# Kernel tuning notes

Hardware: AMD Instinct MI355X
Metric: run time of the kernel (lower is better)

Reference implementation:

```python
import jax, jax.numpy as jnp
import numpy as np

T, B, H, D = 128, 8, 8, 64


def setup_inputs() -> dict:
    key = jax.random.key(0)
    kA, kB, kS = jax.random.split(key, 3)
    # Gated-delta transition matrices: near-identity contractions so the
    # length-T matrix-product recurrence is numerically stable, mimicking
    # A_t = gamma_t * (I - beta_t k_t k_t^T) of the gated delta rule.
    eye = jnp.eye(D, dtype=jnp.float32)
    A = 0.9 * eye + 0.06 * jax.random.normal(kA, (T, B, H, D, D), dtype=jnp.float32)
    Bm = jax.random.normal(kB, (T, B, H, D, D), dtype=jnp.float32)
    init_state = jax.random.normal(kS, (B, H, D, D), dtype=jnp.float32)
    return {"A": A, "Bm": Bm, "init_state": init_state}


def reference(A, Bm, init_state):
    """Gated delta rule recurrence S_t = S_{t-1} @ A_t + B_t for all t,
    computed with a parallel associative scan (Blelloch-equivalent).

    A:  [T,B,H,D,D] transition matrices
    Bm: [T,B,H,D,D] additive updates
    init_state: [B,H,D,D]
    returns states: [T,B,H,D,D]
    """
    def combine(e1, e2):
        # apply e1 first, then e2:
        # (S A1 + B1) A2 + B2 = S (A1 A2) + (B1 A2 + B2)
        A1, B1 = e1
        A2, B2 = e2
        A12 = jnp.einsum('tbhij,tbhjk->tbhik', A1, A2)
        B12 = jnp.einsum('tbhij,tbhjk->tbhik', B1, A2) + B2
        return (A12, B12)

    cumA, cumB = jax.lax.associative_scan(combine, (A, Bm), axis=0)
    # S_t = init_state @ cumA_t + cumB_t
    states = jnp.einsum('bhij,tbhjk->tbhik', init_state, cumA) + cumB
    return states
```

## Files before the change

### kernel.cpp

```cpp
#include <hip/hip_runtime.h>


constexpr int kT = 128;
constexpr int kBH = 64;
constexpr int kD = 64;
constexpr int kTile = kD * kD;

typedef __attribute__((ext_vector_type(8))) short short8;
typedef __attribute__((ext_vector_type(4))) short short4v;
typedef __attribute__((ext_vector_type(4))) float f32x4;

__device__ __forceinline__ unsigned short f2bf(float f) {
  unsigned int u = __float_as_uint(f);
  u += 0x7FFFu + ((u >> 16) & 1u);
  return (unsigned short)(u >> 16);
}
__device__ __forceinline__ float bf2f(unsigned short h) {
  return __uint_as_float(((unsigned int)h) << 16);
}
__device__ __forceinline__ int swzi(int r, int c) { return (r * 64 + c) ^ ((r & 7) << 3); }

__device__ __forceinline__ f32x4 mfma16(short8 a, short8 b, f32x4 c) {
  return __builtin_amdgcn_mfma_f32_16x16x32_bf16(a, b, c, 0, 0, 0);
}

__device__ __forceinline__ void split4(const f32x4 v, short4v& h, short4v& l) {
#pragma unroll
  for (int i = 0; i < 4; ++i) {
    const unsigned short hh = f2bf(v[i]);
    h[i] = (short)hh;
    l[i] = (short)f2bf(v[i] - bf2f(hh));
  }
}

__global__ __launch_bounds__(256, 2) void gdr_fold(
    const float* __restrict__ srcA, const float* __restrict__ srcB,
    float* __restrict__ dstA, float* __restrict__ dstB,
    int perChain, long chainBase, long idxBase, long elemStride, int nElem) {
  __shared__ unsigned short sAh[4096], sAl[4096];
  __shared__ unsigned short sPAh[4096], sPAl[4096];
  __shared__ unsigned short sPBh[4096], sPBl[4096];

  const int tid = threadIdx.x;
  const int lane = tid & 63, wave = tid >> 6;
  const int wr = wave >> 1, wc = wave & 1;
  const int q = lane >> 4, l15 = lane & 15;
  const int bh = blockIdx.x / perChain, id = blockIdx.x % perChain;
  const long e0 = (long)bh * chainBase + (long)id * idxBase;
  const int an = lane, akb = wave;

  f32x4 apa[2][2], apb[2][2];
  {
    const float* At = srcA + (size_t)e0 * kTile;
    const float* Bt = srcB + (size_t)e0 * kTile;
#pragma unroll
    for (int mi = 0; mi < 2; ++mi)
#pragma unroll
      for (int ni = 0; ni < 2; ++ni) {
        const int off = (wc * 32 + ni * 16 + l15) * 64 + wr * 32 + mi * 16 + q * 4;
        apa[mi][ni] = *reinterpret_cast<const f32x4*>(At + off);
        apb[mi][ni] = *reinterpret_cast<const f32x4*>(Bt + off);
      }
  }

  float pfA[16];
  f32x4 pfB[2][2];
  {
    const float* At = srcA + (size_t)(e0 + elemStride) * kTile;
    const float* Bt = srcB + (size_t)(e0 + elemStride) * kTile;
#pragma unroll
    for (int kk = 0; kk < 16; ++kk) pfA[kk] = At[(akb * 16 + kk) * 64 + an];
#pragma unroll
    for (int mi = 0; mi < 2; ++mi)
#pragma unroll
      for (int ni = 0; ni < 2; ++ni)
        pfB[mi][ni] = *reinterpret_cast<const f32x4*>(
            Bt + (wc * 32 + ni * 16 + l15) * 64 + wr * 32 + mi * 16 + q * 4);
  }

  for (int i = 1; i < nElem; ++i) {
    if (i > 1) __syncthreads();
#pragma unroll
    for (int mi = 0; mi < 2; ++mi)
#pragma unroll
      for (int ni = 0; ni < 2; ++ni) {
        const int b = wc * 32 + ni * 16 + l15;
        const int a0 = wr * 32 + mi * 16 + q * 4;
        const int idx = swzi(b, a0);
        short4v h, l;
        split4(apa[mi][ni], h, l);
        *reinterpret_cast<short4v*>(&sPAh[idx]) = h;
        *reinterpret_cast<short4v*>(&sPAl[idx]) = l;
        split4(apb[mi][ni], h, l);
        *reinterpret_cast<short4v*>(&sPBh[idx]) = h;
        *reinterpret_cast<short4v*>(&sPBl[idx]) = l;
      }
#pragma unroll
    for (int s = 0; s < 2; ++s) {
      short8 h, l;
#pragma unroll
      for (int j = 0; j < 8; ++j) {
        const float v = pfA[s * 8 + j];
        const unsigned short hh = f2bf(v);
        h[j] = (short)hh;
        l[j] = (short)f2bf(v - bf2f(hh));
      }
      const int idx = swzi(an, akb * 16 + s * 8);
      *reinterpret_cast<short8*>(&sAh[idx]) = h;
      *reinterpret_cast<short8*>(&sAl[idx]) = l;
    }
    __syncthreads();

#pragma unroll
    for (int mi = 0; mi < 2; ++mi)
#pragma unroll
      for (int ni = 0; ni < 2; ++ni) {
        apa[mi][ni] = (f32x4){0.f, 0.f, 0.f, 0.f};
        apb[mi][ni] = pfB[mi][ni];
      }

    const int in = (i + 1 < nElem) ? i + 1 : i;
    {
      const float* At = srcA + (size_t)(e0 + (long)in * elemStride) * kTile;
      const float* Bt = srcB + (size_t)(e0 + (long)in * elemStride) * kTile;
#pragma unroll
      for (int kk = 0; kk < 16; ++kk) pfA[kk] = At[(akb * 16 + kk) * 64 + an];
#pragma unroll
      for (int mi = 0; mi < 2; ++mi)
#pragma unroll
        for (int ni = 0; ni < 2; ++ni)
          pfB[mi][ni] = *reinterpret_cast<const f32x4*>(
              Bt + (wc * 32 + ni * 16 + l15) * 64 + wr * 32 + mi * 16 + q * 4);
    }

#pragma unroll
    for (int ks = 0; ks < 2; ++ks) {
      short8 xh[2], xl[2], yah[2], yal[2], ybh[2], ybl[2];
      const int colb = ks * 32 + q * 8;
#pragma unroll
      for (int mi = 0; mi < 2; ++mi) {
        const int idx = swzi(wr * 32 + mi * 16 + l15, colb);
        xh[mi] = *reinterpret_cast<const short8*>(&sAh[idx]);
        xl[mi] = *reinterpret_cast<const short8*>(&sAl[idx]);
      }
#pragma unroll
      for (int ni = 0; ni < 2; ++ni) {
        const int idx = swzi(wc * 32 + ni * 16 + l15, colb);
        yah[ni] = *reinterpret_cast<const short8*>(&sPAh[idx]);
        yal[ni] = *reinterpret_cast<const short8*>(&sPAl[idx]);
        ybh[ni] = *reinterpret_cast<const short8*>(&sPBh[idx]);
        ybl[ni] = *reinterpret_cast<const short8*>(&sPBl[idx]);
      }
#pragma unroll
      for (int mi = 0; mi < 2; ++mi)
#pragma unroll
        for (int ni = 0; ni < 2; ++ni) {
          apa[mi][ni] = mfma16(xh[mi], yah[ni], apa[mi][ni]);
          apa[mi][ni] = mfma16(xh[mi], yal[ni], apa[mi][ni]);
          apa[mi][ni] = mfma16(xl[mi], yah[ni], apa[mi][ni]);
          apb[mi][ni] = mfma16(xh[mi], ybh[ni], apb[mi][ni]);
          apb[mi][ni] = mfma16(xh[mi], ybl[ni], apb[mi][ni]);
          apb[mi][ni] = mfma16(xl[mi], ybh[ni], apb[mi][ni]);
        }
    }
  }

  float* pao = dstA + (size_t)blockIdx.x * kTile;
  float* pbo = dstB + (size_t)blockIdx.x * kTile;
#pragma unroll
  for (int mi = 0; mi < 2; ++mi)
#pragma unroll
    for (int ni = 0; ni < 2; ++ni) {
      const int off = (wc * 32 + ni * 16 + l15) * 64 + wr * 32 + mi * 16 + q * 4;
      *reinterpret_cast<f32x4*>(pao + off) = apa[mi][ni];
      *reinterpret_cast<f32x4*>(pbo + off) = apb[mi][ni];
    }
}

__global__ __launch_bounds__(256, 2) void gdr_scan(
    const float* __restrict__ srcA, const float* __restrict__ srcB,
    const float* __restrict__ S0, float* __restrict__ out,
    int perChain, long chainBase, long idxBase, long elemStride,
    int nSteps, int tbMul, int tStep) {
  __shared__ unsigned short sAh[4096], sAl[4096];
  __shared__ unsigned short sSh[4096], sSl[4096];

  const int tid = threadIdx.x;
  const int lane = tid & 63, wave = tid >> 6;
  const int wr = wave >> 1, wc = wave & 1;
  const int q = lane >> 4, l15 = lane & 15;
  const int bh = blockIdx.x / perChain, id = blockIdx.x % perChain;
  const long e0 = (long)bh * chainBase + (long)id * idxBase;
  const int tBase = id * tbMul;
  const int an = lane, akb = wave;

  f32x4 acc[2][2];
  {
    const float* Sb = (tBase == 0) ? (S0 + (size_t)bh * kTile)
                                   : (out + ((size_t)(tBase - 1) * kBH + bh) * kTile);
#pragma unroll
    for (int mi = 0; mi < 2; ++mi)
#pragma unroll
      for (int ni = 0; ni < 2; ++ni)
        acc[mi][ni] = *reinterpret_cast<const f32x4*>(
            Sb + (wc * 32 + ni * 16 + l15) * 64 + wr * 32 + mi * 16 + q * 4);
  }

  float pfA[16];
  f32x4 pfB[2][2];
  {
    const float* At = srcA + (size_t)e0 * kTile;
    const float* Bt = srcB + (size_t)e0 * kTile;
#pragma unroll
    for (int kk = 0; kk < 16; ++kk) pfA[kk] = At[(akb * 16 + kk) * 64 + an];
#pragma unroll
    for (int mi = 0; mi < 2; ++mi)
#pragma unroll
      for (int ni = 0; ni < 2; ++ni)
        pfB[mi][ni] = *reinterpret_cast<const f32x4*>(
            Bt + (wc * 32 + ni * 16 + l15) * 64 + wr * 32 + mi * 16 + q * 4);
  }

  for (int i = 0; i < nSteps; ++i) {
    if (i) __syncthreads();
#pragma unroll
    for (int mi = 0; mi < 2; ++mi)
#pragma unroll
      for (int ni = 0; ni < 2; ++ni) {
        const int b = wc * 32 + ni * 16 + l15;
        const int a0 = wr * 32 + mi * 16 + q * 4;
        const int idx = swzi(b, a0);
        short4v h, l;
        split4(acc[mi][ni], h, l);
        *reinterpret_cast<short4v*>(&sSh[idx]) = h;
        *reinterpret_cast<short4v*>(&sSl[idx]) = l;
      }
#pragma unroll
    for (int s = 0; s < 2; ++s) {
      short8 h, l;
#pragma unroll
      for (int j = 0; j < 8; ++j) {
        const float v = pfA[s * 8 + j];
        const unsigned short hh = f2bf(v);
        h[j] = (short)hh;
        l[j] = (short)f2bf(v - bf2f(hh));
      }
      const int idx = swzi(an, akb * 16 + s * 8);
      *reinterpret_cast<short8*>(&sAh[idx]) = h;
      *reinterpret_cast<short8*>(&sAl[idx]) = l;
    }
    __syncthreads();

#pragma unroll
    for (int mi = 0; mi < 2; ++mi)
#pragma unroll
      for (int ni = 0; ni < 2; ++ni)
        acc[mi][ni] = pfB[mi][ni];

    const int in = (i + 1 < nSteps) ? i + 1 : i;
    {
      const float* At = srcA + (size_t)(e0 + (long)in * elemStride) * kTile;
      const float* Bt = srcB + (size_t)(e0 + (long)in * elemStride) * kTile;
#pragma unroll
      for (int kk = 0; kk < 16; ++kk) pfA[kk] = At[(akb * 16 + kk) * 64 + an];
#pragma unroll
      for (int mi = 0; mi < 2; ++mi)
#pragma unroll
        for (int ni = 0; ni < 2; ++ni)
          pfB[mi][ni] = *reinterpret_cast<const f32x4*>(
              Bt + (wc * 32 + ni * 16 + l15) * 64 + wr * 32 + mi * 16 + q * 4);
    }

#pragma unroll
    for (int ks = 0; ks < 2; ++ks) {
      short8 xh[2], xl[2], yh[2], yl[2];
      const int colb = ks * 32 + q * 8;
#pragma unroll
      for (int mi = 0; mi < 2; ++mi) {
        const int idx = swzi(wr * 32 + mi * 16 + l15, colb);
        xh[mi] = *reinterpret_cast<const short8*>(&sAh[idx]);
        xl[mi] = *reinterpret_cast<const short8*>(&sAl[idx]);
      }
#pragma unroll
      for (int ni = 0; ni < 2; ++ni) {
        const int idx = swzi(wc * 32 + ni * 16 + l15, colb);
        yh[ni] = *reinterpret_cast<const short8*>(&sSh[idx]);
        yl[ni] = *reinterpret_cast<const short8*>(&sSl[idx]);
      }
#pragma unroll
      for (int mi = 0; mi < 2; ++mi)
#pragma unroll
        for (int ni = 0; ni < 2; ++ni) {
          acc[mi][ni] = mfma16(xh[mi], yh[ni], acc[mi][ni]);
          acc[mi][ni] = mfma16(xh[mi], yl[ni], acc[mi][ni]);
          acc[mi][ni] = mfma16(xl[mi], yh[ni], acc[mi][ni]);
        }
    }

    const int t = tBase + (i + 1) * tStep - 1;
    float* o = out + ((size_t)t * kBH + bh) * kTile;
#pragma unroll
    for (int mi = 0; mi < 2; ++mi)
#pragma unroll
      for (int ni = 0; ni < 2; ++ni) {
        const int off = (wc * 32 + ni * 16 + l15) * 64 + wr * 32 + mi * 16 + q * 4;
        *reinterpret_cast<f32x4*>(o + off) = acc[mi][ni];
      }
  }
}

extern "C" void kernel_launch(void* const* d_in, const int* in_sizes, int n_in,
                              void* d_out, int out_size, void* d_ws, size_t ws_size,
                              hipStream_t stream) {
  const float* A  = (const float*)d_in[0];
  const float* Bm = (const float*)d_in[1];
  const float* S0 = (const float*)d_in[2];
  float* out = (float*)d_out;

  int NC;
  if (ws_size >= (size_t)5120 * kTile * 4)      NC = 32;
  else if (ws_size >= (size_t)2560 * kTile * 4) NC = 16;
  else                                          NC = 8;
  const int CH = kT / NC;
  const int NG = NC / 4;

  float* PA = (float*)d_ws;
  float* PB = PA + (size_t)kBH * NC * kTile;
  float* GA = PB + (size_t)kBH * NC * kTile;
  float* GB = GA + (size_t)kBH * NG * kTile;

  gdr_fold<<<dim3(kBH * NC), dim3(256), 0, stream>>>(
      A, Bm, PA, PB, NC, 1L, (long)CH * kBH, (long)kBH, CH);
  gdr_fold<<<dim3(kBH * NG), dim3(256), 0, stream>>>(
      PA, PB, GA, GB, NG, (long)NC, 4L, 1L, 4);
  gdr_scan<<<dim3(kBH), dim3(256), 0, stream>>>(
      GA, GB, S0, out, 1, (long)NG, 0L, 1L, NG, 0, 4 * CH);
  gdr_scan<<<dim3(kBH * NG), dim3(256), 0, stream>>>(
      PA, PB, S0, out, NG, (long)NC, 4L, 1L, 3, 4 * CH, CH);
  gdr_scan<<<dim3(kBH * NC), dim3(256), 0, stream>>>(
      A, Bm, S0, out, NC, 1L, (long)CH * kBH, (long)kBH, CH - 1, CH, 1);
}
```

Baseline: 184.7 us.

## Restructure scan into two-level hierarchy with register-resident state and double-buffered A

```diff
diff --git a/kernel.cpp b/kernel.cpp
--- a/kernel.cpp
+++ b/kernel.cpp
@@ -5,307 +5,251 @@
 constexpr int kBH = 64;
 constexpr int kD = 64;
 constexpr int kTile = kD * kD;
+constexpr int kNC = 16;
+constexpr int kCH = 8;
 
 typedef __attribute__((ext_vector_type(8))) short short8;
-typedef __attribute__((ext_vector_type(4))) short short4v;
 typedef __attribute__((ext_vector_type(4))) float f32x4;
-
-__device__ __forceinline__ unsigned short f2bf(float f) {
-  unsigned int u = __float_as_uint(f);
-  u += 0x7FFFu + ((u >> 16) & 1u);
-  return (unsigned short)(u >> 16);
-}
-__device__ __forceinline__ float bf2f(unsigned short h) {
-  return __uint_as_float(((unsigned int)h) << 16);
-}
+using u32 = unsigned int;
+
+union U8 { u32 u[4]; short8 s; };
+
 __device__ __forceinline__ int swzi(int r, int c) { return (r * 64 + c) ^ ((r & 7) << 3); }
 
 __device__ __forceinline__ f32x4 mfma16(short8 a, short8 b, f32x4 c) {
   return __builtin_amdgcn_mfma_f32_16x16x32_bf16(a, b, c, 0, 0, 0);
 }
 
-__device__ __forceinline__ void split4(const f32x4 v, short4v& h, short4v& l) {
-#pragma unroll
-  for (int i = 0; i < 4; ++i) {
-    const unsigned short hh = f2bf(v[i]);
-    h[i] = (short)hh;
-    l[i] = (short)f2bf(v[i] - bf2f(hh));
-  }
-}
-
-__global__ __launch_bounds__(256, 2) void gdr_fold(
+__device__ __forceinline__ void pk_split(float a, float b, u32& h, u32& l) {
+  u32 hu;
+  asm("v_cvt_pk_bf16_f32 %0, %1, %2" : "=v"(hu) : "v"(a), "v"(b));
+  const float ra = a - __uint_as_float(hu << 16);
+  const float rb = b - __uint_as_float(hu & 0xffff0000u);
+  u32 lu;
+  asm("v_cvt_pk_bf16_f32 %0, %1, %2" : "=v"(lu) : "v"(ra), "v"(rb));
+  h = hu;
+  l = lu;
+}
+
+__device__ __forceinline__ short8 gather_frag(u32 p01, u32 p23, u32 q01, u32 q23,
+                                              int ad0, int ad1, bool lowh) {
+  U8 r;
+  int x, y;
+  x = __builtin_amdgcn_ds_bpermute(ad0, (int)p01);
+  y = __builtin_amdgcn_ds_bpermute(ad0, (int)q01);
+  r.u[0] = (u32)(lowh ? x : y);
+  x = __builtin_amdgcn_ds_bpermute(ad0, (int)p23);
+  y = __builtin_amdgcn_ds_bpermute(ad0, (int)q23);
+  r.u[1] = (u32)(lowh ? x : y);
+  x = __builtin_amdgcn_ds_bpermute(ad1, (int)p01);
+  y = __builtin_amdgcn_ds_bpermute(ad1, (int)q01);
+  r.u[2] = (u32)(lowh ? x : y);
+  x = __builtin_amdgcn_ds_bpermute(ad1, (int)p23);
+  y = __builtin_amdgcn_ds_bpermute(ad1, (int)q23);
+  r.u[3] = (u32)(lowh ? x : y);
+  return r.s;
+}
+
+__device__ __forceinline__ void load_pfA(float* pfA, const float* At, int lane, int w) {
+#pragma unroll
+  for (int kk = 0; kk < 16; ++kk) pfA[kk] = At[(w * 16 + kk) * 64 + lane];
+}
+__device__ __forceinline__ void load_pfB(f32x4* pfB, const float* Bt, int rowbase, int q) {
+#pragma unroll
+  for (int cm = 0; cm < 4; ++cm)
+    pfB[cm] = *reinterpret_cast<const f32x4*>(Bt + rowbase + cm * 16 + q * 4);
+}
+
+__device__ __forceinline__ void stage_A(unsigned short* Ah, unsigned short* Al,
+                                        const float* pfA, int lane, int w) {
+#pragma unroll
+  for (int s = 0; s < 2; ++s) {
+    U8 h, l;
+#pragma unroll
+    for (int p = 0; p < 4; ++p) {
+      u32 hu, lu;
+      pk_split(pfA[s * 8 + 2 * p], pfA[s * 8 + 2 * p + 1], hu, lu);
+      h.u[p] = hu;
+      l.u[p] = lu;
+    }
+    const int idx = swzi(lane, w * 16 + s * 8);
+    *reinterpret_cast<short8*>(&Ah[idx]) = h.s;
+    *reinterpret_cast<short8*>(&Al[idx]) = l.s;
+  }
+}
+
+__global__ __launch_bounds__(256, 3) void gdr_fold(
     const float* __restrict__ srcA, const float* __restrict__ srcB,
     float* __restrict__ dstA, float* __restrict__ dstB,
     int perChain, long chainBase, long idxBase, long elemStride, int nElem) {
-  __shared__ unsigned short sAh[4096], sAl[4096];
-  __shared__ unsigned short sPAh[4096], sPAl[4096];
-  __shared__ unsigned short sPBh[4096], sPBl[4096];
+  __shared__ unsigned short sAh[2][4096], sAl[2][4096];
 
   const int tid = threadIdx.x;
-  const int lane = tid & 63, wave = tid >> 6;
-  const int wr = wave >> 1, wc = wave & 1;
+  const int lane = tid & 63, w = tid >> 6;
   const int q = lane >> 4, l15 = lane & 15;
   const int bh = blockIdx.x / perChain, id = blockIdx.x % perChain;
   const long e0 = (long)bh * chainBase + (long)id * idxBase;
-  const int an = lane, akb = wave;
-
-  f32x4 apa[2][2], apb[2][2];
+  const int rowbase = (w * 16 + l15) * 64;
+  const int ad0 = (l15 + ((lane >> 4) & 1) * 32) * 4;
+  const int ad1 = ad0 + 64;
+  const bool lowh = lane < 32;
+  const int nS = nElem - 1;
+
+  f32x4 apa[4], apb[4];
   {
     const float* At = srcA + (size_t)e0 * kTile;
     const float* Bt = srcB + (size_t)e0 * kTile;
 #pragma unroll
-    for (int mi = 0; mi < 2; ++mi)
-#pragma unroll
-      for (int ni = 0; ni < 2; ++ni) {
-        const int off = (wc * 32 + ni * 16 + l15) * 64 + wr * 32 + mi * 16 + q * 4;
-        apa[mi][ni] = *reinterpret_cast<const f32x4*>(At + off);
-        apb[mi][ni] = *reinterpret_cast<const f32x4*>(Bt + off);
+    for (int cm = 0; cm < 4; ++cm) {
+      apa[cm] = *reinterpret_cast<const f32x4*>(At + rowbase + cm * 16 + q * 4);
+      apb[cm] = *reinterpret_cast<const f32x4*>(Bt + rowbase + cm * 16 + q * 4);
+    }
+  }
+
+  float pfA[16];
+  f32x4 pfB[4];
+  load_pfA(pfA, srcA + (size_t)(e0 + elemStride) * kTile, lane, w);
+  stage_A(sAh[0], sAl[0], pfA, lane, w);
+  __syncthreads();
+  {
+    const long e2 = e0 + (long)(nS > 1 ? 2 : 1) * elemStride;
+    load_pfA(pfA, srcA + (size_t)e2 * kTile, lane, w);
+    load_pfB(pfB, srcB + (size_t)(e0 + elemStride) * kTile, rowbase, q);
+  }
+
+  for (int j = 0; j < nS; ++j) {
+    const int cur = j & 1;
+    f32x4 npa[4], npb[4];
+#pragma unroll
+    for (int cm = 0; cm < 4; ++cm) {
+      npa[cm] = (f32x4){0.f, 0.f, 0.f, 0.f};
+      npb[cm] = pfB[cm];
+    }
+#pragma unroll
+    for (int ks = 0; ks < 2; ++ks) {
+      u32 pa01h, pa01l, pa23h, pa23l, qa01h, qa01l, qa23h, qa23l;
+      u32 pb01h, pb01l, pb23h, pb23l, qb01h, qb01l, qb23h, qb23l;
+      pk_split(apa[2 * ks][0], apa[2 * ks][1], pa01h, pa01l);
+      pk_split(apa[2 * ks][2], apa[2 * ks][3], pa23h, pa23l);
+      pk_split(apa[2 * ks + 1][0], apa[2 * ks + 1][1], qa01h, qa01l);
+      pk_split(apa[2 * ks + 1][2], apa[2 * ks + 1][3], qa23h, qa23l);
+      pk_split(apb[2 * ks][0], apb[2 * ks][1], pb01h, pb01l);
+      pk_split(apb[2 * ks][2], apb[2 * ks][3], pb23h, pb23l);
+      pk_split(apb[2 * ks + 1][0], apb[2 * ks + 1][1], qb01h, qb01l);
+      pk_split(apb[2 * ks + 1][2], apb[2 * ks + 1][3], qb23h, qb23l);
+      const short8 bah = gather_frag(pa01h, pa23h, qa01h, qa23h, ad0, ad1, lowh);
+      const short8 bal = gather_frag(pa01l, pa23l, qa01l, qa23l, ad0, ad1, lowh);
+      const short8 bbh = gather_frag(pb01h, pb23h, qb01h, qb23h, ad0, ad1, lowh);
+      const short8 bbl = gather_frag(pb01l, pb23l, qb01l, qb23l, ad0, ad1, lowh);
+#pragma unroll
+      for (int cm = 0; cm < 4; ++cm) {
+        const int ai = swzi(cm * 16 + l15, ks * 32 + q * 8);
+        const short8 ah = *reinterpret_cast<const short8*>(&sAh[cur][ai]);
+        const short8 al = *reinterpret_cast<const short8*>(&sAl[cur][ai]);
+        npa[cm] = mfma16(ah, bah, npa[cm]);
+        npa[cm] = mfma16(ah, bal, npa[cm]);
+        npa[cm] = mfma16(al, bah, npa[cm]);
+        npb[cm] = mfma16(ah, bbh, npb[cm]);
+        npb[cm] = mfma16(ah, bbl, npb[cm]);
+        npb[cm] = mfma16(al, bbh, npb[cm]);
       }
-  }
-
-  float pfA[16];
-  f32x4 pfB[2][2];
-  {
-    const float* At = srcA + (size_t)(e0 + elemStride) * kTile;
-    const float* Bt = srcB + (size_t)(e0 + elemStride) * kTile;
-#pragma unroll
-    for (int kk = 0; kk < 16; ++kk) pfA[kk] = At[(akb * 16 + kk) * 64 + an];
-#pragma unroll
-    for (int mi = 0; mi < 2; ++mi)
-#pragma unroll
-      for (int ni = 0; ni < 2; ++ni)
-        pfB[mi][ni] = *reinterpret_cast<const f32x4*>(
-            Bt + (wc * 32 + ni * 16 + l15) * 64 + wr * 32 + mi * 16 + q * 4);
-  }
-
-  for (int i = 1; i < nElem; ++i) {
-    if (i > 1) __syncthreads();
-#pragma unroll
-    for (int mi = 0; mi < 2; ++mi)
-#pragma unroll
-      for (int ni = 0; ni < 2; ++ni) {
-        const int b = wc * 32 + ni * 16 + l15;
-        const int a0 = wr * 32 + mi * 16 + q * 4;
-        const int idx = swzi(b, a0);
-        short4v h, l;
-        split4(apa[mi][ni], h, l);
-        *reinterpret_cast<short4v*>(&sPAh[idx]) = h;
-        *reinterpret_cast<short4v*>(&sPAl[idx]) = l;
-        split4(apb[mi][ni], h, l);
-        *reinterpret_cast<short4v*>(&sPBh[idx]) = h;
-        *reinterpret_cast<short4v*>(&sPBl[idx]) = l;
-      }
-#pragma unroll
-    for (int s = 0; s < 2; ++s) {
-      short8 h, l;
-#pragma unroll
-      for (int j = 0; j < 8; ++j) {
-        const float v = pfA[s * 8 + j];
-        const unsigned short hh = f2bf(v);
-        h[j] = (short)hh;
-        l[j] = (short)f2bf(v - bf2f(hh));
-      }
-      const int idx = swzi(an, akb * 16 + s * 8);
-      *reinterpret_cast<short8*>(&sAh[idx]) = h;
-      *reinterpret_cast<short8*>(&sAl[idx]) = l;
-    }
-    __syncthreads();
-
-#pragma unroll
-    for (int mi = 0; mi < 2; ++mi)
-#pragma unroll
-      for (int ni = 0; ni < 2; ++ni) {
-        apa[mi][ni] = (f32x4){0.f, 0.f, 0.f, 0.f};
-        apb[mi][ni] = pfB[mi][ni];
-      }
-
-    const int in = (i + 1 < nElem) ? i + 1 : i;
-    {
-      const float* At = srcA + (size_t)(e0 + (long)in * elemStride) * kTile;
-      const float* Bt = srcB + (size_t)(e0 + (long)in * elemStride) * kTile;
-#pragma unroll
-      for (int kk = 0; kk < 16; ++kk) pfA[kk] = At[(akb * 16 + kk) * 64 + an];
-#pragma unroll
-      for (int mi = 0; mi < 2; ++mi)
-#pragma unroll
-        for (int ni = 0; ni < 2; ++ni)
-          pfB[mi][ni] = *reinterpret_cast<const f32x4*>(
-              Bt + (wc * 32 + ni * 16 + l15) * 64 + wr * 32 + mi * 16 + q * 4);
-    }
-
-#pragma unroll
-    for (int ks = 0; ks < 2; ++ks) {
-      short8 xh[2], xl[2], yah[2], yal[2], ybh[2], ybl[2];
-      const int colb = ks * 32 + q * 8;
-#pragma unroll
-      for (int mi = 0; mi < 2; ++mi) {
-        const int idx = swzi(wr * 32 + mi * 16 + l15, colb);
-        xh[mi] = *reinterpret_cast<const short8*>(&sAh[idx]);
-        xl[mi] = *reinterpret_cast<const short8*>(&sAl[idx]);
-      }
-#pragma unroll
-      for (int ni = 0; ni < 2; ++ni) {
-        const int idx = swzi(wc * 32 + ni * 16 + l15, colb);
-        yah[ni] = *reinterpret_cast<const short8*>(&sPAh[idx]);
-        yal[ni] = *reinterpret_cast<const short8*>(&sPAl[idx]);
-        ybh[ni] = *reinterpret_cast<const short8*>(&sPBh[idx]);
-        ybl[ni] = *reinterpret_cast<const short8*>(&sPBl[idx]);
-      }
-#pragma unroll
-      for (int mi = 0; mi < 2; ++mi)
-#pragma unroll
-        for (int ni = 0; ni < 2; ++ni) {
-          apa[mi][ni] = mfma16(xh[mi], yah[ni], apa[mi][ni]);
-          apa[mi][ni] = mfma16(xh[mi], yal[ni], apa[mi][ni]);
-          apa[mi][ni] = mfma16(xl[mi], yah[ni], apa[mi][ni]);
-          apb[mi][ni] = mfma16(xh[mi], ybh[ni], apb[mi][ni]);
-          apb[mi][ni] = mfma16(xh[mi], ybl[ni], apb[mi][ni]);
-          apb[mi][ni] = mfma16(xl[mi], ybh[ni], apb[mi][ni]);
-        }
-    }
+    }
+    if (j + 1 < nS) {
+      stage_A(sAh[cur ^ 1], sAl[cur ^ 1], pfA, lane, w);
+      const int ja = (j + 3 <= nS) ? j + 3 : nS;
+      load_pfA(pfA, srcA + (size_t)(e0 + (long)ja * elemStride) * kTile, lane, w);
+      load_pfB(pfB, srcB + (size_t)(e0 + (long)(j + 2) * elemStride) * kTile, rowbase, q);
+    }
+#pragma unroll
+    for (int cm = 0; cm < 4; ++cm) { apa[cm] = npa[cm]; apb[cm] = npb[cm]; }
+    if (j + 1 < nS) __syncthreads();
   }
 
   float* pao = dstA + (size_t)blockIdx.x * kTile;
   float* pbo = dstB + (size_t)blockIdx.x * kTile;
 #pragma unroll
-  for (int mi = 0; mi < 2; ++mi)
-#pragma unroll
-    for (int ni = 0; ni < 2; ++ni) {
-      const int off = (wc * 32 + ni * 16 + l15) * 64 + wr * 32 + mi * 16 + q * 4;
-      *reinterpret_cast<f32x4*>(pao + off) = apa[mi][ni];
-      *reinterpret_cast<f32x4*>(pbo + off) = apb[mi][ni];
-    }
-}
-
-__global__ __launch_bounds__(256, 2) void gdr_scan(
+  for (int cm = 0; cm < 4; ++cm) {
+    *reinterpret_cast<f32x4*>(pao + rowbase + cm * 16 + q * 4) = apa[cm];
+    *reinterpret_cast<f32x4*>(pbo + rowbase + cm * 16 + q * 4) = apb[cm];
+  }
+}
+
+__global__ __launch_bounds__(256, 4) void gdr_scan(
     const float* __restrict__ srcA, const float* __restrict__ srcB,
     const float* __restrict__ S0, float* __restrict__ out,
     int perChain, long chainBase, long idxBase, long elemStride,
     int nSteps, int tbMul, int tStep) {
-  __shared__ unsigned short sAh[4096], sAl[4096];
-  __shared__ unsigned short sSh[4096], sSl[4096];
+  __shared__ unsigned short sAh[2][4096], sAl[2][4096];
 
   const int tid = threadIdx.x;
-  const int lane = tid & 63, wave = tid >> 6;
-  const int wr = wave >> 1, wc = wave & 1;
+  const int lane = tid & 63, w = tid >> 6;
   const int q = lane >> 4, l15 = lane & 15;
   const int bh = blockIdx.x / perChain, id = blockIdx.x % perChain;
   const long e0 = (long)bh * chainBase + (long)id * idxBase;
   const int tBase = id * tbMul;
-  const int an = lane, akb = wave;
-
-  f32x4 acc[2][2];
+  const int rowbase = (w * 16 + l15) * 64;
+  const int ad0 = (l15 + ((lane >> 4) & 1) * 32) * 4;
+  const int ad1 = ad0 + 64;
+  const bool lowh = lane < 32;
+
+  f32x4 acc[4];
   {
     const float* Sb = (tBase == 0) ? (S0 + (size_t)bh * kTile)
                                    : (out + ((size_t)(tBase - 1) * kBH + bh) * kTile);
 #pragma unroll
-    for (int mi = 0; mi < 2; ++mi)
-#pragma unroll
-      for (int ni = 0; ni < 2; ++ni)
-        acc[mi][ni] = *reinterpret_cast<const f32x4*>(
-            Sb + (wc * 32 + ni * 16 + l15) * 64 + wr * 32 + mi * 16 + q * 4);
+    for (int cm = 0; cm < 4; ++cm)
+      acc[cm] = *reinterpret_cast<const f32x4*>(Sb + rowbase + cm * 16 + q * 4);
   }
 
   float pfA[16];
-  f32x4 pfB[2][2];
-  {
-    const float* At = srcA + (size_t)e0 * kTile;
-    const float* Bt = srcB + (size_t)e0 * kTile;
-#pragma unroll
-    for (int kk = 0; kk < 16; ++kk) pfA[kk] = At[(akb * 16 + kk) * 64 + an];
-#pragma unroll
-    for (int mi = 0; mi < 2; ++mi)
-#pragma unroll
-      for (int ni = 0; ni < 2; ++ni)
-        pfB[mi][ni] = *reinterpret_cast<const f32x4*>(
-            Bt + (wc * 32 + ni * 16 + l15) * 64 + wr * 32 + mi * 16 + q * 4);
+  f32x4 pfB[4];
+  load_pfA(pfA, srcA + (size_t)e0 * kTile, lane, w);
+  stage_A(sAh[0], sAl[0], pfA, lane, w);
+  __syncthreads();
+  {
+    const long e1 = e0 + (long)(nSteps > 1 ? 1 : 0) * elemStride;
+    load_pfA(pfA, srcA + (size_t)e1 * kTile, lane, w);
+    load_pfB(pfB, srcB + (size_t)e0 * kTile, rowbase, q);
   }
 
   for (int i = 0; i < nSteps; ++i) {
-    if (i) __syncthreads();
-#pragma unroll
-    for (int mi = 0; mi < 2; ++mi)
-#pragma unroll
-      for (int ni = 0; ni < 2; ++ni) {
-        const int b = wc * 32 + ni * 16 + l15;
-        const int a0 = wr * 32 + mi * 16 + q * 4;
-        const int idx = swzi(b, a0);
-        short4v h, l;
-        split4(acc[mi][ni], h, l);
-        *reinterpret_cast<short4v*>(&sSh[idx]) = h;
-        *reinterpret_cast<short4v*>(&sSl[idx]) = l;
+    const int cur = i & 1;
+    f32x4 nacc[4];
+#pragma unroll
+    for (int cm = 0; cm < 4; ++cm) nacc[cm] = pfB[cm];
+#pragma unroll
+    for (int ks = 0; ks < 2; ++ks) {
+      u32 p01h, p01l, p23h, p23l, q01h, q01l, q23h, q23l;
+      pk_split(acc[2 * ks][0], acc[2 * ks][1], p01h, p01l);
+      pk_split(acc[2 * ks][2], acc[2 * ks][3], p23h, p23l);
+      pk_split(acc[2 * ks + 1][0], acc[2 * ks + 1][1], q01h, q01l);
+      pk_split(acc[2 * ks + 1][2], acc[2 * ks + 1][3], q23h, q23l);
+      const short8 bfh = gather_frag(p01h, p23h, q01h, q23h, ad0, ad1, lowh);
+      const short8 bfl = gather_frag(p01l, p23l, q01l, q23l, ad0, ad1, lowh);
+#pragma unroll
+      for (int cm = 0; cm < 4; ++cm) {
+        const int ai = swzi(cm * 16 + l15, ks * 32 + q * 8);
+        const short8 ah = *reinterpret_cast<const short8*>(&sAh[cur][ai]);
+        const short8 al = *reinterpret_cast<const short8*>(&sAl[cur][ai]);
+        nacc[cm] = mfma16(ah, bfh, nacc[cm]);
+        nacc[cm] = mfma16(ah, bfl, nacc[cm]);
+        nacc[cm] = mfma16(al, bfh, nacc[cm]);
       }
-#pragma unroll
-    for (int s = 0; s < 2; ++s) {
-      short8 h, l;
-#pragma unroll
-      for (int j = 0; j < 8; ++j) {
-        const float v = pfA[s * 8 + j];
-        const unsigned short hh = f2bf(v);
-        h[j] = (short)hh;
-        l[j] = (short)f2bf(v - bf2f(hh));
-      }
-      const int idx = swzi(an, akb * 16 + s * 8);
-      *reinterpret_cast<short8*>(&sAh[idx]) = h;
-      *reinterpret_cast<short8*>(&sAl[idx]) = l;
-    }
-    __syncthreads();
-
-#pragma unroll
-    for (int mi = 0; mi < 2; ++mi)
-#pragma unroll
-      for (int ni = 0; ni < 2; ++ni)
-        acc[mi][ni] = pfB[mi][ni];
-
-    const int in = (i + 1 < nSteps) ? i + 1 : i;
-    {
-      const float* At = srcA + (size_t)(e0 + (long)in * elemStride) * kTile;
-      const float* Bt = srcB + (size_t)(e0 + (long)in * elemStride) * kTile;
-#pragma unroll
-      for (int kk = 0; kk < 16; ++kk) pfA[kk] = At[(akb * 16 + kk) * 64 + an];
-#pragma unroll
-      for (int mi = 0; mi < 2; ++mi)
-#pragma unroll
-        for (int ni = 0; ni < 2; ++ni)
-          pfB[mi][ni] = *reinterpret_cast<const f32x4*>(
-              Bt + (wc * 32 + ni * 16 + l15) * 64 + wr * 32 + mi * 16 + q * 4);
-    }
-
-#pragma unroll
-    for (int ks = 0; ks < 2; ++ks) {
-      short8 xh[2], xl[2], yh[2], yl[2];
-      const int colb = ks * 32 + q * 8;
-#pragma unroll
-      for (int mi = 0; mi < 2; ++mi) {
-        const int idx = swzi(wr * 32 + mi * 16 + l15, colb);
-        xh[mi] = *reinterpret_cast<const short8*>(&sAh[idx]);
-        xl[mi] = *reinterpret_cast<const short8*>(&sAl[idx]);
-      }
-#pragma unroll
-      for (int ni = 0; ni < 2; ++ni) {
-        const int idx = swzi(wc * 32 + ni * 16 + l15, colb);
-        yh[ni] = *reinterpret_cast<const short8*>(&sSh[idx]);
-        yl[ni] = *reinterpret_cast<const short8*>(&sSl[idx]);
-      }
-#pragma unroll
-      for (int mi = 0; mi < 2; ++mi)
-#pragma unroll
-        for (int ni = 0; ni < 2; ++ni) {
-          acc[mi][ni] = mfma16(xh[mi], yh[ni], acc[mi][ni]);
-          acc[mi][ni] = mfma16(xh[mi], yl[ni], acc[mi][ni]);
-          acc[mi][ni] = mfma16(xl[mi], yh[ni], acc[mi][ni]);
-        }
-    }
-
+    }
+    if (i + 1 < nSteps) {
+      stage_A(sAh[cur ^ 1], sAl[cur ^ 1], pfA, lane, w);
+      const int ia = (i + 2 <= nSteps - 1) ? i + 2 : nSteps - 1;
+      load_pfA(pfA, srcA + (size_t)(e0 + (long)ia * elemStride) * kTile, lane, w);
+      load_pfB(pfB, srcB + (size_t)(e0 + (long)(i + 1) * elemStride) * kTile, rowbase, q);
+    }
     const int t = tBase + (i + 1) * tStep - 1;
     float* o = out + ((size_t)t * kBH + bh) * kTile;
 #pragma unroll
-    for (int mi = 0; mi < 2; ++mi)
-#pragma unroll
-      for (int ni = 0; ni < 2; ++ni) {
-        const int off = (wc * 32 + ni * 16 + l15) * 64 + wr * 32 + mi * 16 + q * 4;
-        *reinterpret_cast<f32x4*>(o + off) = acc[mi][ni];
-      }
+    for (int cm = 0; cm < 4; ++cm) {
+      *reinterpret_cast<f32x4*>(o + rowbase + cm * 16 + q * 4) = nacc[cm];
+      acc[cm] = nacc[cm];
+    }
+    if (i + 1 < nSteps) __syncthreads();
   }
 }
 
@@ -317,26 +261,13 @@
   const float* S0 = (const float*)d_in[2];
   float* out = (float*)d_out;
 
-  int NC;
-  if (ws_size >= (size_t)5120 * kTile * 4)      NC = 32;
-  else if (ws_size >= (size_t)2560 * kTile * 4) NC = 16;
-  else                                          NC = 8;
-  const int CH = kT / NC;
-  const int NG = NC / 4;
-
   float* PA = (float*)d_ws;
-  float* PB = PA + (size_t)kBH * NC * kTile;
-  float* GA = PB + (size_t)kBH * NC * kTile;
-  float* GB = GA + (size_t)kBH * NG * kTile;
-
-  gdr_fold<<<dim3(kBH * NC), dim3(256), 0, stream>>>(
-      A, Bm, PA, PB, NC, 1L, (long)CH * kBH, (long)kBH, CH);
-  gdr_fold<<<dim3(kBH * NG), dim3(256), 0, stream>>>(
-      PA, PB, GA, GB, NG, (long)NC, 4L, 1L, 4);
+  float* PB = PA + (size_t)kBH * kNC * kTile;
+
+  gdr_fold<<<dim3(kBH * kNC), dim3(256), 0, stream>>>(
+      A, Bm, PA, PB, kNC, 1L, (long)kCH * kBH, (long)kBH, kCH);
   gdr_scan<<<dim3(kBH), dim3(256), 0, stream>>>(
-      GA, GB, S0, out, 1, (long)NG, 0L, 1L, NG, 0, 4 * CH);
-  gdr_scan<<<dim3(kBH * NG), dim3(256), 0, stream>>>(
-      PA, PB, S0, out, NG, (long)NC, 4L, 1L, 3, 4 * CH, CH);
-  gdr_scan<<<dim3(kBH * NC), dim3(256), 0, stream>>>(
-      A, Bm, S0, out, NC, 1L, (long)CH * kBH, (long)kBH, CH - 1, CH, 1);
-}
+      PA, PB, S0, out, 1, (long)kNC, 0L, 1L, kNC, 0, kCH);
+  gdr_scan<<<dim3(kBH * kNC), dim3(256), 0, stream>>>(
+      A, Bm, S0, out, kNC, 1L, (long)kCH * kBH, (long)kBH, kCH - 1, kCH, 1);
+}
```

Result: faster. 159.2 us (-13.8%).
